# Optimization experiments

Measured on AMD Instinct MI355X. Metric: run time of the kernel, lower is better.

The kernel has to match this reference:

```python
import jax, jax.numpy as jnp
import numpy as np

EPS = 1e-6

def _phi(x):
    # elu(x) + 1 feature map
    return jax.nn.elu(x) + 1.0

def setup_inputs() -> dict:
    key = jax.random.key(0)
    kq, kk, kv = jax.random.split(key, 3)
    N, L, S, H, D, M = 8, 4096, 4096, 8, 64, 64
    queries = jax.random.normal(kq, (N, L, H, D), dtype=jnp.float32)
    keys = jax.random.normal(kk, (N, S, H, D), dtype=jnp.float32)
    values = jax.random.normal(kv, (N, S, H, M), dtype=jnp.float32)
    key_mask = jnp.ones((N, S), dtype=jnp.float32)  # key_lengths.float_matrix
    return {"queries": queries, "keys": keys, "values": values, "key_mask": key_mask}

def reference(queries, keys, values, key_mask):
    Q = _phi(queries)                                   # [N,L,H,D]
    K = _phi(keys) * key_mask[:, :, None, None]         # [N,S,H,D]
    KV = jnp.einsum('nshd,nshm->nhmd', K, values)       # [N,H,M,D]
    Z = 1.0 / (jnp.einsum('nlhd,nhd->nlh', Q, K.sum(axis=1)) + EPS)  # [N,L,H]
    V = jnp.einsum('nlhd,nhmd,nlh->nlhm', Q, KV, Z)     # [N,L,H,M]
    return V
```

## Files before the change

kernel.cpp:

```cpp
#include <hip/hip_runtime.h>


#define SLEN 4096
#define LLEN 4096
#define NB   8
#define HH   8
#define DD   64
#define MM   64
#define HD   512

__device__ __forceinline__ float phi(float x) {
    return x > 0.0f ? x + 1.0f : __expf(x);
}

__device__ __forceinline__ void fma4(float4& a, float s, float4 b) {
    a.x = fmaf(s, b.x, a.x);
    a.y = fmaf(s, b.y, a.y);
    a.z = fmaf(s, b.z, a.z);
    a.w = fmaf(s, b.w, a.w);
}

__global__ __launch_bounds__(256)
void la_phase1(const float* __restrict__ Kg, const float* __restrict__ Vg,
               const float* __restrict__ maskg,
               float* __restrict__ KVt, float* __restrict__ Ksum) {
    __shared__ float Ks[64 * 64];
    __shared__ float Vs[64 * 64];
    __shared__ float Red[64 * 68];
    __shared__ float KsB[16 * 64];

    const int tid  = threadIdx.x;
    const int nh   = blockIdx.y;
    const int n    = nh >> 3;
    const int h    = nh & 7;
    const int sbase = blockIdx.x * 512;

    const size_t base = (size_t)n * SLEN * HD + (size_t)h * DD;
    const float* mrow = maskg + (size_t)n * SLEN;

    const int col4 = (tid & 15) * 4;
    const int r0   = tid >> 4;

    const int lane = tid & 63;
    const int grp  = tid >> 6;
    const int d0   = (lane & 7) * 8;
    const int m0   = (lane >> 3) * 8;

    float4 acc[8][2];
    #pragma unroll
    for (int i = 0; i < 8; ++i) {
        acc[i][0] = make_float4(0.f, 0.f, 0.f, 0.f);
        acc[i][1] = make_float4(0.f, 0.f, 0.f, 0.f);
    }
    float4 ksp = make_float4(0.f, 0.f, 0.f, 0.f);

    for (int t = 0; t < 8; ++t) {
        const int srow0 = sbase + t * 64;
        #pragma unroll
        for (int rr = 0; rr < 4; ++rr) {
            const int row = r0 + rr * 16;
            const int s   = srow0 + row;
            const size_t goff = base + (size_t)s * HD + col4;
            float4 kf = *(const float4*)(Kg + goff);
            const float mmv = mrow[s];
            kf.x = phi(kf.x) * mmv;
            kf.y = phi(kf.y) * mmv;
            kf.z = phi(kf.z) * mmv;
            kf.w = phi(kf.w) * mmv;
            *(float4*)&Ks[row * 64 + col4] = kf;
            ksp.x += kf.x; ksp.y += kf.y; ksp.z += kf.z; ksp.w += kf.w;
            *(float4*)&Vs[row * 64 + col4] = *(const float4*)(Vg + goff);
        }
        __syncthreads();
        #pragma unroll 4
        for (int s = grp; s < 64; s += 4) {
            float4 ka = *(const float4*)&Ks[s * 64 + d0];
            float4 kb = *(const float4*)&Ks[s * 64 + d0 + 4];
            float4 va = *(const float4*)&Vs[s * 64 + m0];
            float4 vb = *(const float4*)&Vs[s * 64 + m0 + 4];
            const float kk[8] = {ka.x, ka.y, ka.z, ka.w, kb.x, kb.y, kb.z, kb.w};
            #pragma unroll
            for (int di = 0; di < 8; ++di) {
                fma4(acc[di][0], kk[di], va);
                fma4(acc[di][1], kk[di], vb);
            }
        }
        __syncthreads();
    }

    if (grp == 0) {
        #pragma unroll
        for (int di = 0; di < 8; ++di) {
            *(float4*)&Red[(d0 + di) * 68 + m0]     = acc[di][0];
            *(float4*)&Red[(d0 + di) * 68 + m0 + 4] = acc[di][1];
        }
    }
    __syncthreads();
    for (int g = 1; g < 4; ++g) {
        if (grp == g) {
            #pragma unroll
            for (int di = 0; di < 8; ++di) {
                float4* p0 = (float4*)&Red[(d0 + di) * 68 + m0];
                float4* p1 = (float4*)&Red[(d0 + di) * 68 + m0 + 4];
                float4 v0 = *p0, v1 = *p1;
                v0.x += acc[di][0].x; v0.y += acc[di][0].y; v0.z += acc[di][0].z; v0.w += acc[di][0].w;
                v1.x += acc[di][1].x; v1.y += acc[di][1].y; v1.z += acc[di][1].z; v1.w += acc[di][1].w;
                *p0 = v0; *p1 = v1;
            }
        }
        __syncthreads();
    }

    *(float4*)&KsB[r0 * 64 + col4] = ksp;
    __syncthreads();
    if (tid < 64) {
        float ssum = 0.f;
        #pragma unroll
        for (int r = 0; r < 16; ++r) ssum += KsB[r * 64 + tid];
        atomicAdd(&Ksum[nh * 64 + tid], ssum);
    }

    for (int k2 = 0; k2 < 16; ++k2) {
        const int idx = k2 * 256 + tid;
        atomicAdd(&KVt[(size_t)nh * 4096 + idx], Red[(idx >> 6) * 68 + (idx & 63)]);
    }
}

__global__ __launch_bounds__(128)
void la_phase2(const float* __restrict__ Qg, const float* __restrict__ KVt,
               const float* __restrict__ Ksum, float* __restrict__ Og) {
    __shared__ float Qs[128 * 68];
    __shared__ float KVs[64 * 64];
    __shared__ float KSs[64];

    const int tid = threadIdx.x;
    const int nh  = blockIdx.y;
    const int n   = nh >> 3;
    const int h   = nh & 7;
    const int lbase = blockIdx.x * 128;

    const int col4 = (tid & 15) * 4;
    const int r0   = tid >> 4;
    #pragma unroll
    for (int rr = 0; rr < 16; ++rr) {
        const int row = r0 + rr * 8;
        const int l   = lbase + row;
        float4 q = *(const float4*)&Qg[((size_t)(n * LLEN + l) * HH + h) * DD + col4];
        q.x = phi(q.x); q.y = phi(q.y); q.z = phi(q.z); q.w = phi(q.w);
        *(float4*)&Qs[row * 68 + col4] = q;
    }
    #pragma unroll
    for (int k2 = 0; k2 < 8; ++k2) {
        const int f = k2 * 128 + tid;
        *(float4*)&KVs[f * 4] = *(const float4*)&KVt[(size_t)nh * 4096 + f * 4];
    }
    if (tid < 16) *(float4*)&KSs[tid * 4] = *(const float4*)&Ksum[nh * 64 + tid * 4];
    __syncthreads();

    const int wv   = tid >> 6;
    const int lane = tid & 63;
    const int tx   = lane & 7;
    const int ty   = lane >> 3;
    const int rowbase = wv * 64 + ty;
    const int m0 = tx * 8;

    float4 acc[8][2];
    float  den[8];
    #pragma unroll
    for (int i = 0; i < 8; ++i) {
        acc[i][0] = make_float4(0.f, 0.f, 0.f, 0.f);
        acc[i][1] = make_float4(0.f, 0.f, 0.f, 0.f);
        den[i] = 0.f;
    }

    for (int d4 = 0; d4 < 16; ++d4) {
        float4 q4[8];
        #pragma unroll
        for (int i = 0; i < 8; ++i)
            q4[i] = *(const float4*)&Qs[(rowbase + 8 * i) * 68 + d4 * 4];
        const float4 ks = *(const float4*)&KSs[d4 * 4];
        #pragma unroll
        for (int i = 0; i < 8; ++i) {
            den[i] = fmaf(q4[i].x, ks.x, den[i]);
            den[i] = fmaf(q4[i].y, ks.y, den[i]);
            den[i] = fmaf(q4[i].z, ks.z, den[i]);
            den[i] = fmaf(q4[i].w, ks.w, den[i]);
        }
        #pragma unroll
        for (int dk = 0; dk < 4; ++dk) {
            const int d = d4 * 4 + dk;
            const float4 kv0 = *(const float4*)&KVs[d * 64 + m0];
            const float4 kv1 = *(const float4*)&KVs[d * 64 + m0 + 4];
            #pragma unroll
            for (int i = 0; i < 8; ++i) {
                const float qs = ((const float*)&q4[i])[dk];
                fma4(acc[i][0], qs, kv0);
                fma4(acc[i][1], qs, kv1);
            }
        }
    }

    #pragma unroll
    for (int i = 0; i < 8; ++i) {
        const int l = lbase + rowbase + 8 * i;
        const float z = 1.0f / (den[i] + 1e-6f);
        float4 o0 = acc[i][0], o1 = acc[i][1];
        o0.x *= z; o0.y *= z; o0.z *= z; o0.w *= z;
        o1.x *= z; o1.y *= z; o1.z *= z; o1.w *= z;
        const size_t off = ((size_t)(n * LLEN + l) * HH + h) * MM + m0;
        *(float4*)&Og[off]     = o0;
        *(float4*)&Og[off + 4] = o1;
    }
}

extern "C" void kernel_launch(void* const* d_in, const int* in_sizes, int n_in,
                              void* d_out, int out_size, void* d_ws, size_t ws_size,
                              hipStream_t stream) {
    const float* Q    = (const float*)d_in[0];
    const float* K    = (const float*)d_in[1];
    const float* V    = (const float*)d_in[2];
    const float* mask = (const float*)d_in[3];
    float* out  = (float*)d_out;
    float* KVt  = (float*)d_ws;
    float* Ksum = KVt + (size_t)NB * HH * DD * MM;

    hipMemsetAsync(d_ws, 0, ((size_t)NB * HH * DD * MM + (size_t)NB * HH * DD) * sizeof(float), stream);

    dim3 g1(SLEN / 512, NB * HH);
    la_phase1<<<g1, 256, 0, stream>>>(K, V, mask, KVt, Ksum);

    dim3 g2(LLEN / 128, NB * HH);
    la_phase2<<<g2, 128, 0, stream>>>(Q, KVt, Ksum, out);
}
```

Baseline: 262.7 us.

## Replace atomic KV accumulation with split partials plus reduce kernel; retile both phases

Phase 1 now splits S into 16 chunks of 256 rows per head and writes per-split partial KV and Ksum buffers instead of atomically adding into a zeroed workspace. A separate reduce kernel sums those partials, which removes the memset and the atomics. Phase 1 also drops the cross-wave shared-memory reduction by giving each wave a distinct 32x32 quadrant. Phase 2 moves to 256 threads, each computing 8 rows by 4 columns. This doubles the phase-1 block count and cuts per-thread registers, at the cost of an extra kernel launch and partial-buffer traffic.

```diff
diff --git a/kernel.cpp b/kernel.cpp
--- a/kernel.cpp
+++ b/kernel.cpp
@@ -3,17 +3,16 @@
 
 #define SLEN 4096
 #define LLEN 4096
-#define NB   8
-#define HH   8
-#define DD   64
-#define MM   64
+#define NHTOT 64
 #define HD   512
+#define NSPLIT 16
+#define EPSF 1e-6f
 
 __device__ __forceinline__ float phi(float x) {
     return x > 0.0f ? x + 1.0f : __expf(x);
 }
 
-__device__ __forceinline__ void fma4(float4& a, float s, float4 b) {
+__device__ __forceinline__ void fma4(float4& a, float s, const float4& b) {
     a.x = fmaf(s, b.x, a.x);
     a.y = fmaf(s, b.y, a.y);
     a.z = fmaf(s, b.z, a.z);
@@ -23,110 +22,105 @@
 __global__ __launch_bounds__(256)
 void la_phase1(const float* __restrict__ Kg, const float* __restrict__ Vg,
                const float* __restrict__ maskg,
-               float* __restrict__ KVt, float* __restrict__ Ksum) {
-    __shared__ float Ks[64 * 64];
-    __shared__ float Vs[64 * 64];
-    __shared__ float Red[64 * 68];
-    __shared__ float KsB[16 * 64];
+               float* __restrict__ KVp, float* __restrict__ Ksump) {
+    __shared__ float kb[64 * 68];
+    __shared__ float vb[64 * 64];
+    __shared__ float ksb[16 * 64];
 
     const int tid  = threadIdx.x;
+    const int w    = tid >> 6;
+    const int lane = tid & 63;
     const int nh   = blockIdx.y;
     const int n    = nh >> 3;
     const int h    = nh & 7;
-    const int sbase = blockIdx.x * 512;
-
-    const size_t base = (size_t)n * SLEN * HD + (size_t)h * DD;
+    const int sp   = blockIdx.x;
+
+    const int sr = tid >> 4;
+    const int c4 = (tid & 15) * 4;
+    const int wd = w & 1, wm = w >> 1;
+    const int d0 = wd * 32 + (lane & 7) * 4;
+    const int m0 = wm * 32 + (lane >> 3) * 4;
+
+    const size_t base = (size_t)n * SLEN * HD + (size_t)h * 64;
     const float* mrow = maskg + (size_t)n * SLEN;
-
-    const int col4 = (tid & 15) * 4;
-    const int r0   = tid >> 4;
-
-    const int lane = tid & 63;
-    const int grp  = tid >> 6;
-    const int d0   = (lane & 7) * 8;
-    const int m0   = (lane >> 3) * 8;
-
-    float4 acc[8][2];
-    #pragma unroll
-    for (int i = 0; i < 8; ++i) {
-        acc[i][0] = make_float4(0.f, 0.f, 0.f, 0.f);
-        acc[i][1] = make_float4(0.f, 0.f, 0.f, 0.f);
-    }
+    const int sblock = sp * 256;
+
+    float4 acc[4];
+    #pragma unroll
+    for (int i = 0; i < 4; ++i) acc[i] = make_float4(0.f, 0.f, 0.f, 0.f);
     float4 ksp = make_float4(0.f, 0.f, 0.f, 0.f);
 
-    for (int t = 0; t < 8; ++t) {
-        const int srow0 = sbase + t * 64;
-        #pragma unroll
-        for (int rr = 0; rr < 4; ++rr) {
-            const int row = r0 + rr * 16;
+    for (int t = 0; t < 4; ++t) {
+        const int srow0 = sblock + t * 64;
+        __syncthreads();
+        #pragma unroll
+        for (int u = 0; u < 4; ++u) {
+            const int row = sr + u * 16;
             const int s   = srow0 + row;
-            const size_t goff = base + (size_t)s * HD + col4;
-            float4 kf = *(const float4*)(Kg + goff);
-            const float mmv = mrow[s];
-            kf.x = phi(kf.x) * mmv;
-            kf.y = phi(kf.y) * mmv;
-            kf.z = phi(kf.z) * mmv;
-            kf.w = phi(kf.w) * mmv;
-            *(float4*)&Ks[row * 64 + col4] = kf;
+            const size_t g = base + (size_t)s * HD + c4;
+            float4 kf = *(const float4*)(Kg + g);
+            const float mm = mrow[s];
+            kf.x = phi(kf.x) * mm;
+            kf.y = phi(kf.y) * mm;
+            kf.z = phi(kf.z) * mm;
+            kf.w = phi(kf.w) * mm;
             ksp.x += kf.x; ksp.y += kf.y; ksp.z += kf.z; ksp.w += kf.w;
-            *(float4*)&Vs[row * 64 + col4] = *(const float4*)(Vg + goff);
+            *(float4*)&kb[row * 68 + c4] = kf;
+            *(float4*)&vb[row * 64 + c4] = *(const float4*)(Vg + g);
         }
         __syncthreads();
-        #pragma unroll 4
-        for (int s = grp; s < 64; s += 4) {
-            float4 ka = *(const float4*)&Ks[s * 64 + d0];
-            float4 kb = *(const float4*)&Ks[s * 64 + d0 + 4];
-            float4 va = *(const float4*)&Vs[s * 64 + m0];
-            float4 vb = *(const float4*)&Vs[s * 64 + m0 + 4];
-            const float kk[8] = {ka.x, ka.y, ka.z, ka.w, kb.x, kb.y, kb.z, kb.w};
-            #pragma unroll
-            for (int di = 0; di < 8; ++di) {
-                fma4(acc[di][0], kk[di], va);
-                fma4(acc[di][1], kk[di], vb);
-            }
-        }
-        __syncthreads();
-    }
-
-    if (grp == 0) {
-        #pragma unroll
-        for (int di = 0; di < 8; ++di) {
-            *(float4*)&Red[(d0 + di) * 68 + m0]     = acc[di][0];
-            *(float4*)&Red[(d0 + di) * 68 + m0 + 4] = acc[di][1];
-        }
-    }
-    __syncthreads();
-    for (int g = 1; g < 4; ++g) {
-        if (grp == g) {
-            #pragma unroll
-            for (int di = 0; di < 8; ++di) {
-                float4* p0 = (float4*)&Red[(d0 + di) * 68 + m0];
-                float4* p1 = (float4*)&Red[(d0 + di) * 68 + m0 + 4];
-                float4 v0 = *p0, v1 = *p1;
-                v0.x += acc[di][0].x; v0.y += acc[di][0].y; v0.z += acc[di][0].z; v0.w += acc[di][0].w;
-                v1.x += acc[di][1].x; v1.y += acc[di][1].y; v1.z += acc[di][1].z; v1.w += acc[di][1].w;
-                *p0 = v0; *p1 = v1;
-            }
-        }
-        __syncthreads();
-    }
-
-    *(float4*)&KsB[r0 * 64 + col4] = ksp;
+        #pragma unroll 8
+        for (int s = 0; s < 64; ++s) {
+            const float4 k4 = *(const float4*)&kb[s * 68 + d0];
+            const float4 v4 = *(const float4*)&vb[s * 64 + m0];
+            fma4(acc[0], k4.x, v4);
+            fma4(acc[1], k4.y, v4);
+            fma4(acc[2], k4.z, v4);
+            fma4(acc[3], k4.w, v4);
+        }
+    }
+
+    float* outp = KVp + ((size_t)sp * NHTOT + nh) * 4096;
+    #pragma unroll
+    for (int di = 0; di < 4; ++di)
+        *(float4*)&outp[(d0 + di) * 64 + m0] = acc[di];
+
+    *(float4*)&ksb[sr * 64 + c4] = ksp;
     __syncthreads();
     if (tid < 64) {
         float ssum = 0.f;
         #pragma unroll
-        for (int r = 0; r < 16; ++r) ssum += KsB[r * 64 + tid];
-        atomicAdd(&Ksum[nh * 64 + tid], ssum);
-    }
-
-    for (int k2 = 0; k2 < 16; ++k2) {
-        const int idx = k2 * 256 + tid;
-        atomicAdd(&KVt[(size_t)nh * 4096 + idx], Red[(idx >> 6) * 68 + (idx & 63)]);
-    }
-}
-
-__global__ __launch_bounds__(128)
+        for (int r = 0; r < 16; ++r) ssum += ksb[r * 64 + tid];
+        Ksump[((size_t)sp * NHTOT + nh) * 64 + tid] = ssum;
+    }
+}
+
+__global__ __launch_bounds__(256)
+void la_reduce(const float* __restrict__ KVp, const float* __restrict__ Ksump,
+               float* __restrict__ KVt, float* __restrict__ Ksum) {
+    const int nh  = blockIdx.x;
+    const int tid = threadIdx.x;
+    #pragma unroll
+    for (int j = 0; j < 4; ++j) {
+        const int f = (j * 256 + tid) * 4;
+        float4 a = make_float4(0.f, 0.f, 0.f, 0.f);
+        #pragma unroll
+        for (int s = 0; s < NSPLIT; ++s) {
+            const float4 v = *(const float4*)&KVp[((size_t)s * NHTOT + nh) * 4096 + f];
+            a.x += v.x; a.y += v.y; a.z += v.z; a.w += v.w;
+        }
+        *(float4*)&KVt[(size_t)nh * 4096 + f] = a;
+    }
+    if (tid < 64) {
+        float a = 0.f;
+        #pragma unroll
+        for (int s = 0; s < NSPLIT; ++s)
+            a += Ksump[((size_t)s * NHTOT + nh) * 64 + tid];
+        Ksum[nh * 64 + tid] = a;
+    }
+}
+
+__global__ __launch_bounds__(256)
 void la_phase2(const float* __restrict__ Qg, const float* __restrict__ KVt,
                const float* __restrict__ Ksum, float* __restrict__ Og) {
     __shared__ float Qs[128 * 68];
@@ -139,46 +133,45 @@
     const int h   = nh & 7;
     const int lbase = blockIdx.x * 128;
 
-    const int col4 = (tid & 15) * 4;
-    const int r0   = tid >> 4;
-    #pragma unroll
-    for (int rr = 0; rr < 16; ++rr) {
-        const int row = r0 + rr * 8;
-        const int l   = lbase + row;
-        float4 q = *(const float4*)&Qg[((size_t)(n * LLEN + l) * HH + h) * DD + col4];
+    #pragma unroll
+    for (int j = 0; j < 4; ++j) {
+        const int f = (j * 256 + tid) * 4;
+        *(float4*)&KVs[f] = *(const float4*)&KVt[(size_t)nh * 4096 + f];
+    }
+    if (tid < 16) *(float4*)&KSs[tid * 4] = *(const float4*)&Ksum[nh * 64 + tid * 4];
+
+    const int sr = tid >> 4;
+    const int c4 = (tid & 15) * 4;
+    #pragma unroll
+    for (int u = 0; u < 8; ++u) {
+        const int row = sr + u * 16;
+        float4 q = *(const float4*)&Qg[((size_t)(n * LLEN + lbase + row) * 8 + h) * 64 + c4];
         q.x = phi(q.x); q.y = phi(q.y); q.z = phi(q.z); q.w = phi(q.w);
-        *(float4*)&Qs[row * 68 + col4] = q;
-    }
-    #pragma unroll
-    for (int k2 = 0; k2 < 8; ++k2) {
-        const int f = k2 * 128 + tid;
-        *(float4*)&KVs[f * 4] = *(const float4*)&KVt[(size_t)nh * 4096 + f * 4];
-    }
-    if (tid < 16) *(float4*)&KSs[tid * 4] = *(const float4*)&Ksum[nh * 64 + tid * 4];
+        *(float4*)&Qs[row * 68 + c4] = q;
+    }
     __syncthreads();
 
-    const int wv   = tid >> 6;
+    const int w    = tid >> 6;
     const int lane = tid & 63;
-    const int tx   = lane & 7;
-    const int ty   = lane >> 3;
-    const int rowbase = wv * 64 + ty;
-    const int m0 = tx * 8;
-
-    float4 acc[8][2];
+    const int ty   = lane >> 4;
+    const int tx   = lane & 15;
+    const int m0   = tx * 4;
+    const int rb   = w * 32 + ty;
+
+    float4 acc[8];
     float  den[8];
     #pragma unroll
     for (int i = 0; i < 8; ++i) {
-        acc[i][0] = make_float4(0.f, 0.f, 0.f, 0.f);
-        acc[i][1] = make_float4(0.f, 0.f, 0.f, 0.f);
+        acc[i] = make_float4(0.f, 0.f, 0.f, 0.f);
         den[i] = 0.f;
     }
 
     for (int d4 = 0; d4 < 16; ++d4) {
+        const float4 ks = *(const float4*)&KSs[d4 * 4];
         float4 q4[8];
         #pragma unroll
         for (int i = 0; i < 8; ++i)
-            q4[i] = *(const float4*)&Qs[(rowbase + 8 * i) * 68 + d4 * 4];
-        const float4 ks = *(const float4*)&KSs[d4 * 4];
+            q4[i] = *(const float4*)&Qs[(rb + 4 * i) * 68 + d4 * 4];
         #pragma unroll
         for (int i = 0; i < 8; ++i) {
             den[i] = fmaf(q4[i].x, ks.x, den[i]);
@@ -188,28 +181,20 @@
         }
         #pragma unroll
         for (int dk = 0; dk < 4; ++dk) {
-            const int d = d4 * 4 + dk;
-            const float4 kv0 = *(const float4*)&KVs[d * 64 + m0];
-            const float4 kv1 = *(const float4*)&KVs[d * 64 + m0 + 4];
+            const float4 kv = *(const float4*)&KVs[(d4 * 4 + dk) * 64 + m0];
             #pragma unroll
-            for (int i = 0; i < 8; ++i) {
-                const float qs = ((const float*)&q4[i])[dk];
-                fma4(acc[i][0], qs, kv0);
-                fma4(acc[i][1], qs, kv1);
-            }
+            for (int i = 0; i < 8; ++i)
+                fma4(acc[i], (&q4[i].x)[dk], kv);
         }
     }
 
     #pragma unroll
     for (int i = 0; i < 8; ++i) {
-        const int l = lbase + rowbase + 8 * i;
-        const float z = 1.0f / (den[i] + 1e-6f);
-        float4 o0 = acc[i][0], o1 = acc[i][1];
-        o0.x *= z; o0.y *= z; o0.z *= z; o0.w *= z;
-        o1.x *= z; o1.y *= z; o1.z *= z; o1.w *= z;
-        const size_t off = ((size_t)(n * LLEN + l) * HH + h) * MM + m0;
-        *(float4*)&Og[off]     = o0;
-        *(float4*)&Og[off + 4] = o1;
+        const int l = lbase + rb + 4 * i;
+        const float z = 1.0f / (den[i] + EPSF);
+        float4 o = acc[i];
+        o.x *= z; o.y *= z; o.z *= z; o.w *= z;
+        *(float4*)&Og[((size_t)(n * LLEN + l) * 8 + h) * 64 + m0] = o;
     }
 }
 
@@ -220,15 +205,18 @@
     const float* K    = (const float*)d_in[1];
     const float* V    = (const float*)d_in[2];
     const float* mask = (const float*)d_in[3];
-    float* out  = (float*)d_out;
-    float* KVt  = (float*)d_ws;
-    float* Ksum = KVt + (size_t)NB * HH * DD * MM;
-
-    hipMemsetAsync(d_ws, 0, ((size_t)NB * HH * DD * MM + (size_t)NB * HH * DD) * sizeof(float), stream);
-
-    dim3 g1(SLEN / 512, NB * HH);
-    la_phase1<<<g1, 256, 0, stream>>>(K, V, mask, KVt, Ksum);
-
-    dim3 g2(LLEN / 128, NB * HH);
-    la_phase2<<<g2, 128, 0, stream>>>(Q, KVt, Ksum, out);
-}
+    float* out = (float*)d_out;
+
+    float* KVp   = (float*)d_ws;
+    float* Ksump = KVp + (size_t)NSPLIT * NHTOT * 4096;
+    float* KVt   = Ksump + (size_t)NSPLIT * NHTOT * 64;
+    float* Ksum  = KVt + (size_t)NHTOT * 4096;
+
+    dim3 g1(NSPLIT, NHTOT);
+    la_phase1<<<g1, 256, 0, stream>>>(K, V, mask, KVp, Ksump);
+
+    la_reduce<<<NHTOT, 256, 0, stream>>>(KVp, Ksump, KVt, Ksum);
+
+    dim3 g2(LLEN / 128, NHTOT);
+    la_phase2<<<g2, 256, 0, stream>>>(Q, KVt, Ksum, out);
+}
```

Result: faster. 255.1 us (-2.9%).
